# Optimization experiments

Measured on AMD Instinct MI355X. Metric: run time of the kernel, lower is better.

The kernel has to match this reference:

```python
import jax, jax.numpy as jnp
import numpy as np

HEADS = 8
HEAD_DIM = 64
INNER = HEADS * HEAD_DIM  # 512
DIM = 512
B, H, W = 8, 32, 32
KV_LEN, KV_DIM = 77, 1024


def group_norm(x, g, b, groups=32, eps=1e-6):
    # x: [B, C, H, W]
    Bx, C, Hx, Wx = x.shape
    xr = x.reshape(Bx, groups, C // groups, Hx, Wx)
    mu = xr.mean(axis=(2, 3, 4), keepdims=True)
    var = xr.var(axis=(2, 3, 4), keepdims=True)
    xr = (xr - mu) * jax.lax.rsqrt(var + eps)
    return xr.reshape(Bx, C, Hx, Wx) * g[None, :, None, None] + b[None, :, None, None]


def layer_norm(x, g, b, eps=1e-5):
    mu = x.mean(axis=-1, keepdims=True)
    var = x.var(axis=-1, keepdims=True)
    return (x - mu) * jax.lax.rsqrt(var + eps) * g + b


def attention(qx, kvx, Wq, Wk, Wv, Wo, bo):
    # qx: [B, Sq, dim_q], kvx: [B, Sk, dim_kv]
    q = qx @ Wq
    k = kvx @ Wk
    v = kvx @ Wv
    Bx, Sq, _ = q.shape
    Sk = k.shape[1]
    q = q.reshape(Bx, Sq, HEADS, HEAD_DIM)
    k = k.reshape(Bx, Sk, HEADS, HEAD_DIM)
    v = v.reshape(Bx, Sk, HEADS, HEAD_DIM)
    att = jnp.einsum('bqhd,bkhd->bhqk', q, k) * (HEAD_DIM ** -0.5)
    att = jax.nn.softmax(att.astype(jnp.float32), axis=-1).astype(q.dtype)
    o = jnp.einsum('bhqk,bkhd->bqhd', att, v).reshape(Bx, Sq, INNER)
    return o @ Wo + bo


def setup_inputs() -> dict:
    key = jax.random.key(0)
    ks = jax.random.split(key, 20)
    s = 0.02
    def n(k, shape):
        return jax.random.normal(k, shape, jnp.float32) * s
    return {
        'q': jax.random.normal(ks[0], (B, DIM, H, W), jnp.float32),
        'kv': jax.random.normal(ks[1], (B, KV_LEN, KV_DIM), jnp.float32),
        'gn_g': jnp.ones((DIM,), jnp.float32), 'gn_b': jnp.zeros((DIM,), jnp.float32),
        'ln2_g': jnp.ones((INNER,), jnp.float32), 'ln2_b': jnp.zeros((INNER,), jnp.float32),
        'ln3_g': jnp.ones((INNER,), jnp.float32), 'ln3_b': jnp.zeros((INNER,), jnp.float32),
        'ln4_g': jnp.ones((INNER,), jnp.float32), 'ln4_b': jnp.zeros((INNER,), jnp.float32),
        'fc_in_w': n(ks[2], (DIM, INNER)), 'fc_in_b': jnp.zeros((INNER,), jnp.float32),
        'fc_out_w': n(ks[3], (INNER, DIM)), 'fc_out_b': jnp.zeros((DIM,), jnp.float32),
        'a1_q': n(ks[4], (INNER, INNER)), 'a1_k': n(ks[5], (INNER, INNER)),
        'a1_v': n(ks[6], (INNER, INNER)), 'a1_o': n(ks[7], (INNER, INNER)),
        'a1_ob': jnp.zeros((INNER,), jnp.float32),
        'a2_q': n(ks[8], (INNER, INNER)), 'a2_k': n(ks[9], (KV_DIM, INNER)),
        'a2_v': n(ks[10], (KV_DIM, INNER)), 'a2_o': n(ks[11], (INNER, INNER)),
        'a2_ob': jnp.zeros((INNER,), jnp.float32),
        'ff_proj_w': n(ks[12], (INNER, INNER * 8)), 'ff_proj_b': jnp.zeros((INNER * 8,), jnp.float32),
        'ff_out_w': n(ks[13], (INNER * 4, INNER)), 'ff_out_b': jnp.zeros((INNER,), jnp.float32),
    }


def reference(q, kv, gn_g, gn_b, ln2_g, ln2_b, ln3_g, ln3_b, ln4_g, ln4_b,
              fc_in_w, fc_in_b, fc_out_w, fc_out_b,
              a1_q, a1_k, a1_v, a1_o, a1_ob,
              a2_q, a2_k, a2_v, a2_o, a2_ob,
              ff_proj_w, ff_proj_b, ff_out_w, ff_out_b):
    res = q
    Bx, C, Hx, Wx = q.shape
    x = group_norm(q, gn_g, gn_b)
    x = x.reshape(Bx, C, Hx * Wx).transpose(0, 2, 1)  # [B, S, C]
    x = x @ fc_in_w + fc_in_b
    t = layer_norm(x, ln2_g, ln2_b)
    x = attention(t, t, a1_q, a1_k, a1_v, a1_o, a1_ob) + x
    x = attention(layer_norm(x, ln3_g, ln3_b), kv, a2_q, a2_k, a2_v, a2_o, a2_ob) + x
    h = layer_norm(x, ln4_g, ln4_b) @ ff_proj_w + ff_proj_b
    a, gate = jnp.split(h, 2, axis=-1)
    x = (a * jax.nn.gelu(gate, approximate=False)) @ ff_out_w + ff_out_b + x
    x = x @ fc_out_w + fc_out_b
    x = x.transpose(0, 2, 1).reshape(Bx, C, Hx, Wx)
    return x + res
```

## Files before the change

### kernel.cpp

```cpp
#include <hip/hip_runtime.h>
#include <cstdint>
#include <cstddef>

typedef __attribute__((ext_vector_type(8))) short bf16x8;
typedef __attribute__((ext_vector_type(4))) short short4v;
typedef __attribute__((ext_vector_type(4))) float f32x4;

__device__ __forceinline__ short f2b(float f) {
    unsigned u = __builtin_bit_cast(unsigned, f);
    u = (u + 0x7FFFu + ((u >> 16) & 1u)) >> 16;
    return (short)u;
}
__device__ __forceinline__ float b2f(short s) {
    unsigned u = ((unsigned)(unsigned short)s) << 16;
    return __builtin_bit_cast(float, u);
}

__device__ __forceinline__ void gload16(const short* g, short* l) {
    __builtin_amdgcn_global_load_lds(
        (const __attribute__((address_space(1))) unsigned int*)g,
        (__attribute__((address_space(3))) unsigned int*)l, 16, 0, 0);
}

__device__ __forceinline__ float gelu_fast(float g) {
    float g2 = g * g;
    float gp = g * (0.7978845608f + 0.0356774081f * g2);
    float t = exp2f(-2.885390082f * gp);
    return g / (1.f + t);
}

__device__ __forceinline__ int pn_ffp(int n) {
    int m = (n < 2048) ? n : (n - 2048);
    int gofs = (n < 2048) ? 0 : 32;
    int x = m >> 6, c = m & 63;
    return x * 128 + ((c >> 5) << 6) + gofs + (c & 31);
}

struct PrepArgs {
    const float* src[12];
    short* dst[12];
    const float* kv;
    short* kvb;
    const float* fb;
    float* bp;
    const float* qin;
    const float* gng;
    const float* gnb;
    float* gnsc;
    float* gnsh;
};

__global__ __launch_bounds__(256) void prep(PrepArgs a) {
    int t = blockIdx.x;
    int tid = threadIdx.x;
    __shared__ float tile[32][33];
    if (t >= 6144) {
        if (t >= 6468) {
            int bb = (t - 6468) >> 5, gg = (t - 6468) & 31;
            const float4* src = (const float4*)(a.qin + ((size_t)(bb * 512 + gg * 16)) * 1024);
            float s = 0.f, s2 = 0.f;
#pragma unroll
            for (int i = 0; i < 16; ++i) {
                float4 v = src[tid + 256 * i];
                s += (v.x + v.y) + (v.z + v.w);
                s2 += (v.x * v.x + v.y * v.y) + (v.z * v.z + v.w * v.w);
            }
#pragma unroll
            for (int m = 1; m < 64; m <<= 1) {
                s += __shfl_xor(s, m);
                s2 += __shfl_xor(s2, m);
            }
            float* red = &tile[0][0];
            int wv = tid >> 6;
            if ((tid & 63) == 0) { red[wv] = s; red[4 + wv] = s2; }
            __syncthreads();
            if (tid < 16) {
                float S = red[0] + red[1] + red[2] + red[3];
                float S2 = red[4] + red[5] + red[6] + red[7];
                float mu = S * (1.f / 16384.f);
                float var = S2 * (1.f / 16384.f) - mu * mu;
                float rs = rsqrtf(var + 1e-6f);
                int c = gg * 16 + tid;
                float scale = rs * a.gng[c];
                a.gnsc[bb * 512 + c] = scale;
                a.gnsh[bb * 512 + c] = a.gnb[c] - mu * scale;
            }
            return;
        }
        if (t >= 6452) {
            int n = (t - 6452) * 256 + tid;
            if (n < 4096) a.bp[pn_ffp(n)] = a.fb[n];
            return;
        }
        int idx = (t - 6144) * 256 + tid;
        if (idx >= 78848) return;
        const float4* s = (const float4*)a.kv + (size_t)idx * 2;
        float4 va = s[0], vb = s[1];
        bf16x8 w;
        w[0] = f2b(va.x); w[1] = f2b(va.y); w[2] = f2b(va.z); w[3] = f2b(va.w);
        w[4] = f2b(vb.x); w[5] = f2b(vb.y); w[6] = f2b(vb.z); w[7] = f2b(vb.w);
        *(bf16x8*)(a.kvb + (size_t)idx * 8) = w;
        return;
    }
    const int jstart[12] = {0, 256, 512, 768, 1024, 1280, 1536, 1792, 2304, 2816, 3072, 5120};
    const int jK[12] = {512, 512, 512, 512, 512, 512, 512, 1024, 1024, 512, 512, 2048};
    const int jN[12] = {512, 512, 512, 512, 512, 512, 512, 512, 512, 512, 4096, 512};
    int j = 11;
#pragma unroll
    for (int i = 11; i >= 1; --i)
        if (t < jstart[i]) j = i - 1;
    int tx = t - jstart[j];
    int K = jK[j], N = jN[j];
    int tn = N >> 5;
    int n0 = (tx % tn) * 32, k0 = (tx / tn) * 32;
    const float* w = a.src[j];
    short* wt = a.dst[j];
    bool perm = (j == 10);

    int cx = tid & 31, ty0 = tid >> 5;
#pragma unroll
    for (int i = 0; i < 4; ++i) {
        int r = ty0 + i * 8;
        tile[r][cx] = w[(size_t)(k0 + r) * N + n0 + cx];
    }
    __syncthreads();
    int r = tid >> 3;
    int kg = (tid & 7) * 4;
    int drow = perm ? pn_ffp(n0 + r) : (n0 + r);
    short4v o = {f2b(tile[kg][r]), f2b(tile[kg + 1][r]),
                 f2b(tile[kg + 2][r]), f2b(tile[kg + 3][r])};
    *(short4v*)&wt[(size_t)drow * K + k0 + kg] = o;
}

__global__ __launch_bounds__(256) void gn_apply(const float* __restrict__ q,
                                                const float* __restrict__ sc,
                                                const float* __restrict__ sh,
                                                short* __restrict__ out) {
    __shared__ short tile[512][33];
    int b = blockIdx.x >> 5, st = blockIdx.x & 31;
    int s0 = st * 32;
    int sl = threadIdx.x & 31, cg = threadIdx.x >> 5;
    for (int c = cg; c < 512; c += 8) {
        float v = q[((size_t)(b * 512 + c)) * 1024 + s0 + sl];
        float y = v * sc[b * 512 + c] + sh[b * 512 + c];
        tile[c][sl] = f2b(y);
    }
    __syncthreads();
    int sr = threadIdx.x >> 3, ch = threadIdx.x & 7;
    short* orow = out + ((size_t)(b * 1024 + s0 + sr)) * 512;
    for (int c8 = ch * 64; c8 < ch * 64 + 64; c8 += 8) {
        bf16x8 o;
#pragma unroll
        for (int jj = 0; jj < 8; ++jj) o[jj] = tile[c8 + jj][sr];
        *(bf16x8*)&orow[c8] = o;
    }
}

__global__ __launch_bounds__(256) void ln_rows(const short* __restrict__ x,
                                               const float* __restrict__ g,
                                               const float* __restrict__ bta,
                                               short* __restrict__ out) {
    int row = blockIdx.x * 4 + (threadIdx.x >> 6);
    int lane = threadIdx.x & 63;
    bf16x8 v8 = *(const bf16x8*)(x + (size_t)row * 512 + lane * 8);
    float v[8];
#pragma unroll
    for (int j = 0; j < 8; ++j) v[j] = b2f(v8[j]);
    float s = 0.f, s2 = 0.f;
#pragma unroll
    for (int j = 0; j < 8; ++j) { s += v[j]; s2 += v[j] * v[j]; }
#pragma unroll
    for (int m = 1; m < 64; m <<= 1) {
        s += __shfl_xor(s, m);
        s2 += __shfl_xor(s2, m);
    }
    float mu = s * (1.f / 512.f);
    float var = s2 * (1.f / 512.f) - mu * mu;
    float rs = rsqrtf(var + 1e-5f);
    float4 ga = ((const float4*)g)[lane * 2], gb = ((const float4*)g)[lane * 2 + 1];
    float4 ba = ((const float4*)bta)[lane * 2], bb = ((const float4*)bta)[lane * 2 + 1];
    bf16x8 o;
    o[0] = f2b((v[0] - mu) * rs * ga.x + ba.x);
    o[1] = f2b((v[1] - mu) * rs * ga.y + ba.y);
    o[2] = f2b((v[2] - mu) * rs * ga.z + ba.z);
    o[3] = f2b((v[3] - mu) * rs * ga.w + ba.w);
    o[4] = f2b((v[4] - mu) * rs * gb.x + bb.x);
    o[5] = f2b((v[5] - mu) * rs * gb.y + bb.y);
    o[6] = f2b((v[6] - mu) * rs * gb.z + bb.z);
    o[7] = f2b((v[7] - mu) * rs * gb.w + bb.w);
    *(bf16x8*)(out + (size_t)row * 512 + lane * 8) = o;
}

template <int BN>
__device__ __forceinline__ void gemm_body(
    short* smem,
    const short* __restrict__ A, const short* __restrict__ BT,
    int M, int N, int K,
    const float* __restrict__ bias,
    const short* __restrict__ addSrcB,
    short* __restrict__ outB,
    const float* __restrict__ resid,
    float* __restrict__ outFinal,
    int mode, int bx, int by) {
    constexpr int FJ = BN / 32;
    constexpr int ASZ = 3 * 128 * 32;
    short* Asb = smem;
    short* Bsb = smem + ASZ;
    int tid = threadIdx.x;
    int wave = tid >> 6, lane = tid & 63;
    int wr = wave >> 1, wc = wave & 1;
    int m0 = by * 128, n0 = bx * BN;
    f32x4 acc[4][FJ];
#pragma unroll
    for (int i = 0; i < 4; ++i)
#pragma unroll
        for (int j = 0; j < FJ; ++j) acc[i][j] = (f32x4){0.f, 0.f, 0.f, 0.f};

    int srow = tid >> 2;
    int scg = (((tid & 3) ^ ((tid >> 3) & 3)) << 3);
    int ar0 = m0 + srow; if (ar0 >= M) ar0 = M - 1;
    int ar1 = m0 + 64 + srow; if (ar1 >= M) ar1 = M - 1;
    const short* ag0 = A + (size_t)ar0 * K + scg;
    const short* ag1 = A + (size_t)ar1 * K + scg;
    const short* bg0 = BT + (size_t)(n0 + srow) * K + scg;
    const short* bg1 = BT + (size_t)(n0 + 64 + srow) * K + scg;
    int nk = K >> 5;

    auto stage = [&](int buf) {
        gload16(ag0, &Asb[buf * 4096 + wave * 512]);
        gload16(ag1, &Asb[buf * 4096 + 2048 + wave * 512]);
        gload16(bg0, &Bsb[buf * (BN * 32) + wave * 512]);
        if constexpr (BN == 128) gload16(bg1, &Bsb[buf * 4096 + 2048 + wave * 512]);
        ag0 += 32; ag1 += 32; bg0 += 32; bg1 += 32;
    };
    stage(0);
    stage(1);

    int lr = lane & 15, g = lane >> 4;

#define GL_STEP(KT, BUF)                                                          \
    {                                                                             \
        __builtin_amdgcn_sched_barrier(0);                                        \
        if ((KT) + 1 < nk) {                                                      \
            if constexpr (BN == 128)                                              \
                asm volatile("s_waitcnt vmcnt(4)" ::: "memory");                  \
            else                                                                  \
                asm volatile("s_waitcnt vmcnt(3)" ::: "memory");                  \
        } else {                                                                  \
            asm volatile("s_waitcnt vmcnt(0)" ::: "memory");                      \
        }                                                                         \
        __builtin_amdgcn_sched_barrier(0);                                        \
        __builtin_amdgcn_s_barrier();                                             \
        if ((KT) + 2 < nk) stage(((BUF) + 2) % 3);                                \
        bf16x8 af[4], bfr[FJ];                                                    \
        _Pragma("unroll") for (int i = 0; i < 4; ++i) {                           \
            int row = wr * 64 + i * 16 + lr;                                      \
            af[i] = *(const bf16x8*)&Asb[(BUF) * 4096 + row * 32 +                \
                                         ((g ^ ((row >> 1) & 3)) << 3)];          \
        }                                                                         \
        _Pragma("unroll") for (int j = 0; j < FJ; ++j) {                          \
            int row = wc * (BN / 2) + j * 16 + lr;                                \
            bfr[j] = *(const bf16x8*)&Bsb[(BUF) * (BN * 32) + row * 32 +          \
                                          ((g ^ ((row >> 1) & 3)) << 3)];         \
        }                                                                         \
        _Pragma("unroll") for (int i = 0; i < 4; ++i)                             \
            _Pragma("unroll") for (int j = 0; j < FJ; ++j)                        \
                acc[i][j] = __builtin_amdgcn_mfma_f32_16x16x32_bf16(              \
                    af[i], bfr[j], acc[i][j], 0, 0, 0);                           \
    }

    for (int kt = 0; kt < nk; kt += 3) {
        GL_STEP(kt, 0);
        if (kt + 1 < nk) GL_STEP(kt + 1, 1);
        if (kt + 2 < nk) GL_STEP(kt + 2, 2);
    }
#undef GL_STEP

    int lq = lane >> 4;
    if (mode == 1) {
#pragma unroll
        for (int i = 0; i < 4; ++i)
#pragma unroll
            for (int j = 0; j < FJ; ++j) {
                int mm0 = m0 + wr * 64 + i * 16 + lq * 4;
                int nn = n0 + wc * (BN / 2) + j * 16 + lr;
                int bb = mm0 >> 10, ss = mm0 & 1023;
                size_t oi = ((size_t)(bb * 512 + nn)) * 1024 + ss;
                float bv = bias ? bias[nn] : 0.f;
                float4 rv = *(const float4*)&resid[oi];
                float4 ov;
                ov.x = acc[i][j][0] + bv + rv.x;
                ov.y = acc[i][j][1] + bv + rv.y;
                ov.z = acc[i][j][2] + bv + rv.z;
                ov.w = acc[i][j][3] + bv + rv.w;
                *(float4*)&outFinal[oi] = ov;
            }
        return;
    }
    {
        constexpr int EC = BN + 4;
        float* ef = (float*)smem;
#pragma unroll
        for (int h = 0; h < 2; ++h) {
            __syncthreads();
            if (wr == h) {
#pragma unroll
                for (int i = 0; i < 4; ++i)
#pragma unroll
                    for (int j = 0; j < FJ; ++j)
#pragma unroll
                        for (int r = 0; r < 4; ++r)
                            ef[(i * 16 + lq * 4 + r) * EC + wc * (BN / 2) + j * 16 + lr] =
                                acc[i][j][r];
            }
            __syncthreads();
#pragma unroll
            for (int q = 0; q < BN / 16; ++q) {
                int idx = q * 256 + tid;
                int row = idx / (BN / 4);
                int cq = (idx % (BN / 4)) * 4;
                int mm = m0 + h * 64 + row;
                if (mm >= M) continue;
                int nn = n0 + cq;
                float4 v = *(float4*)&ef[row * EC + cq];
                if (bias) {
                    float4 b4 = *(const float4*)&bias[nn];
                    v.x += b4.x; v.y += b4.y; v.z += b4.z; v.w += b4.w;
                }
                size_t ig = (size_t)mm * N + nn;
                if (addSrcB) {
                    short4v a4 = *(const short4v*)&addSrcB[ig];
                    v.x += b2f(a4[0]); v.y += b2f(a4[1]);
                    v.z += b2f(a4[2]); v.w += b2f(a4[3]);
                }
                short4v o = {f2b(v.x), f2b(v.y), f2b(v.z), f2b(v.w)};
                *(short4v*)&outB[ig] = o;
            }
        }
    }
}

template <int BN>
__global__ __launch_bounds__(256, 1) void gemm_gl(
    const short* __restrict__ A, const short* __restrict__ BT,
    int M, int N, int K,
    const float* __restrict__ bias,
    const short* __restrict__ addSrcB,
    short* __restrict__ outB,
    const float* __restrict__ resid,
    float* __restrict__ outFinal,
    int mode) {
    __shared__ __attribute__((aligned(16))) short smem[3 * 128 * 32 + 3 * BN * 32];
    gemm_body<BN>(smem, A, BT, M, N, K, bias, addSrcB, outB, resid, outFinal,
                  mode, blockIdx.x, blockIdx.y);
}

__global__ __launch_bounds__(256, 1) void gemm_dual(
    const short* __restrict__ A1, const short* __restrict__ B1,
    short* __restrict__ O1, int M1, int N1, int K1,
    const short* __restrict__ A2, const short* __restrict__ B2,
    short* __restrict__ O2, int M2, int N2, int K2) {
    __shared__ __attribute__((aligned(16))) short smem[3 * 128 * 32 + 3 * 128 * 32];
    int t = blockIdx.x;
    if (t < 80) {
        gemm_body<64>(smem, A2, B2, M2, N2, K2, nullptr, nullptr, O2,
                      nullptr, nullptr, 0, t & 15, t >> 4);
    } else {
        t -= 80;
        gemm_body<128>(smem, A1, B1, M1, N1, K1, nullptr, nullptr, O1,
                       nullptr, nullptr, 0, t & 3, t >> 2);
    }
}

__global__ __launch_bounds__(512, 1) void gemm256w(
    const short* __restrict__ A, const short* __restrict__ BT,
    int M, int N, int K,
    const float* __restrict__ bias,
    const short* __restrict__ addSrcB,
    short* __restrict__ outB,
    int mode) {
    __shared__ __attribute__((aligned(16))) short smem[3 * 4096 + 3 * 8192];
    short* Asb = smem;
    short* Bsb = smem + 12288;
    int tid = threadIdx.x;
    int wave = tid >> 6, lane = tid & 63;
    int wrM = wave >> 2, wcN = wave & 3;
    int m0 = blockIdx.y * 128, n0 = blockIdx.x * 256;
    f32x4 acc[4][4];
#pragma unroll
    for (int i = 0; i < 4; ++i)
#pragma unroll
        for (int j = 0; j < 4; ++j) acc[i][j] = (f32x4){0.f, 0.f, 0.f, 0.f};

    const short* gp[3];
    int ldsoff[3];
    bool isA[3];
#pragma unroll
    for (int s = 0; s < 3; ++s) {
        int qq = wave * 3 + s;
        bool a = qq < 8;
        int r = (a ? qq : qq - 8) * 16 + (lane >> 2);
        int sc = (((lane & 3) ^ ((r >> 1) & 3)) << 3);
        gp[s] = a ? (A + (size_t)(m0 + r) * K + sc)
                  : (BT + (size_t)(n0 + r) * K + sc);
        ldsoff[s] = (a ? qq : (qq - 8)) * 512;
        isA[s] = a;
    }
    int nk = K >> 5;
    auto stage = [&](int buf) {
#pragma unroll
        for (int s = 0; s < 3; ++s) {
            short* l = isA[s] ? &Asb[buf * 4096 + ldsoff[s]]
                              : &Bsb[buf * 8192 + ldsoff[s]];
            gload16(gp[s], l);
            gp[s] += 32;
        }
    };
    stage(0);
    stage(1);

    int lr = lane & 15, g = lane >> 4;

#define W8_STEP(KT, BUF)                                                          \
    {                                                                             \
        __builtin_amdgcn_sched_barrier(0);                                        \
        if ((KT) + 1 < nk) {                                                      \
            asm volatile("s_waitcnt vmcnt(3)" ::: "memory");                      \
        } else {                                                                  \
            asm volatile("s_waitcnt vmcnt(0)" ::: "memory");                      \
        }                                                                         \
        __builtin_amdgcn_sched_barrier(0);                                        \
        __builtin_amdgcn_s_barrier();                                             \
        if ((KT) + 2 < nk) stage(((BUF) + 2) % 3);                                \
        bf16x8 af[4], bfr[4];                                                     \
        _Pragma("unroll") for (int i = 0; i < 4; ++i) {                           \
            int row = wrM * 64 + i * 16 + lr;                                     \
            af[i] = *(const bf16x8*)&Asb[(BUF) * 4096 + row * 32 +                \
                                         ((g ^ ((row >> 1) & 3)) << 3)];          \
        }                                                                         \
        _Pragma("unroll") for (int j = 0; j < 4; ++j) {                           \
            int row = wcN * 64 + j * 16 + lr;                                     \
            bfr[j] = *(const bf16x8*)&Bsb[(BUF) * 8192 + row * 32 +               \
                                          ((g ^ ((row >> 1) & 3)) << 3)];         \
        }                                                                         \
        _Pragma("unroll") for (int i = 0; i < 4; ++i)                             \
            _Pragma("unroll") for (int j = 0; j < 4; ++j)                         \
                acc[i][j] = __builtin_amdgcn_mfma_f32_16x16x32_bf16(              \
                    af[i], bfr[j], acc[i][j], 0, 0, 0);                           \
    }

    for (int kt = 0; kt < nk; kt += 3) {
        W8_STEP(kt, 0);
        if (kt + 1 < nk) W8_STEP(kt + 1, 1);
        if (kt + 2 < nk) W8_STEP(kt + 2, 2);
    }
#undef W8_STEP

    int lq = lane >> 4;
    if (mode == 2) {
        short* eb = smem;
        int xhalf = wcN >> 1, half = wcN & 1;
        __syncthreads();
#pragma unroll
        for (int i = 0; i < 4; ++i)
#pragma unroll
            for (int j = 0; j < 2; ++j)
#pragma unroll
                for (int r = 0; r < 4; ++r) {
                    int slot = n0 + wcN * 64 + j * 16 + lr;
                    float a = acc[i][j][r] + bias[slot];
                    float gt = acc[i][j + 2][r] + bias[slot + 32];
                    float ge = gelu_fast(gt);
                    int row = wrM * 64 + i * 16 + lq * 4 + r;
                    int col = xhalf * 64 + half * 32 + j * 16 + lr;
                    eb[row * 136 + col] = f2b(a * ge);
                }
        __syncthreads();
#pragma unroll
        for (int q = 0; q < 4; ++q) {
            int idx = q * 512 + tid;
            int row = idx >> 4, cg = (idx & 15) * 8;
            bf16x8 o = *(bf16x8*)&eb[row * 136 + cg];
            *(bf16x8*)&outB[(size_t)(m0 + row) * 2048 + blockIdx.x * 128 + cg] = o;
        }
        return;
    }
    {
        float* ef = (float*)smem;
#pragma unroll
        for (int h = 0; h < 2; ++h) {
            __syncthreads();
            if (wrM == h) {
#pragma unroll
                for (int i = 0; i < 4; ++i)
#pragma unroll
                    for (int j = 0; j < 4; ++j)
#pragma unroll
                        for (int r = 0; r < 4; ++r)
                            ef[(i * 16 + lq * 4 + r) * 260 + wcN * 64 + j * 16 + lr] =
                                acc[i][j][r];
            }
            __syncthreads();
#pragma unroll
            for (int q = 0; q < 8; ++q) {
                int idx = q * 512 + tid;
                int row = idx >> 6;
                int cq = (idx & 63) * 4;
                float4 v = *(float4*)&ef[row * 260 + cq];
                int nn = n0 + cq;
                if (bias) {
                    float4 b4 = *(const float4*)&bias[nn];
                    v.x += b4.x; v.y += b4.y; v.z += b4.z; v.w += b4.w;
                }
                size_t ig = (size_t)(m0 + h * 64 + row) * N + nn;
                if (addSrcB) {
                    short4v a4 = *(const short4v*)&addSrcB[ig];
                    v.x += b2f(a4[0]); v.y += b2f(a4[1]);
                    v.z += b2f(a4[2]); v.w += b2f(a4[3]);
                }
                short4v o = {f2b(v.x), f2b(v.y), f2b(v.z), f2b(v.w)};
                *(short4v*)&outB[ig] = o;
            }
        }
    }
}

__global__ __launch_bounds__(256, 1) void attn_mfma(const short* __restrict__ qp,
                                                    const short* __restrict__ kp,
                                                    const short* __restrict__ vp,
                                                    short* __restrict__ op,
                                                    int kv_len, int kvBatchRows,
                                                    int qStride, int kvStride) {
    __shared__ __attribute__((aligned(16))) short Kt[64][72];
    __shared__ __attribute__((aligned(16))) short Vt[64][72];
    __shared__ __attribute__((aligned(16))) short Pt[4][2][16][72];
    int tid = threadIdx.x, w = tid >> 6, lane = tid & 63;
    int g = lane >> 4, c = lane & 15;
    int id = blockIdx.x;
    int xcd = id & 7, jj2 = id >> 3;
    int bh = xcd * 8 + (jj2 >> 3);
    int qtile = jj2 & 7;
    int b = bh >> 3, h = bh & 7;
    int q0 = qtile * 128 + w * 16;

    const float QS = 0.125f * 1.44269504f;
    bf16x8 qa[2][2];
#pragma unroll
    for (int qi = 0; qi < 2; ++qi) {
        const short* qbase = qp + ((size_t)(b * 1024 + q0 + qi * 64 + c)) * qStride + h * 64;
        bf16x8 qr0 = *(const bf16x8*)(qbase + g * 8);
        bf16x8 qr1 = *(const bf16x8*)(qbase + 32 + g * 8);
#pragma unroll
        for (int j = 0; j < 8; ++j) {
            qa[qi][0][j] = f2b(b2f(qr0[j]) * QS);
            qa[qi][1][j] = f2b(b2f(qr1[j]) * QS);
        }
    }
    bf16x8 vones;
#pragma unroll
    for (int j = 0; j < 8; ++j) vones[j] = (short)0x3F80;

    f32x4 oac[2][4], oacl[2];
#pragma unroll
    for (int qi = 0; qi < 2; ++qi) {
#pragma unroll
        for (int dt = 0; dt < 4; ++dt) oac[qi][dt] = (f32x4){0.f, 0.f, 0.f, 0.f};
        oacl[qi] = (f32x4){0.f, 0.f, 0.f, 0.f};
    }

    int skey = tid & 63, sd0 = (tid >> 6) * 16;
    int ntile = (kv_len + 63) >> 6;
    size_t kvbase = (size_t)b * kvBatchRows;

    bf16x8 k0, k1, v0, v1;
    {
        int krow = skey < kv_len ? skey : kv_len - 1;
        const short* kpp = kp + (kvbase + krow) * kvStride + h * 64 + sd0;
        const short* vpp = vp + (kvbase + krow) * kvStride + h * 64 + sd0;
        k0 = *(const bf16x8*)kpp; k1 = *(const bf16x8*)(kpp + 8);
        v0 = *(const bf16x8*)vpp; v1 = *(const bf16x8*)(vpp + 8);
    }

    for (int kt = 0; kt < ntile; ++kt) {
        __syncthreads();
        *(bf16x8*)&Kt[skey][sd0] = k0;
        *(bf16x8*)&Kt[skey][sd0 + 8] = k1;
#pragma unroll
        for (int j = 0; j < 8; ++j) {
            Vt[sd0 + j][skey] = v0[j];
            Vt[sd0 + 8 + j][skey] = v1[j];
        }
        __syncthreads();
        if (kt + 1 < ntile) {
            int krow = (kt + 1) * 64 + skey;
            if (krow >= kv_len) krow = kv_len - 1;
            const short* kpp = kp + (kvbase + krow) * kvStride + h * 64 + sd0;
            const short* vpp = vp + (kvbase + krow) * kvStride + h * 64 + sd0;
            k0 = *(const bf16x8*)kpp; k1 = *(const bf16x8*)(kpp + 8);
            v0 = *(const bf16x8*)vpp; v1 = *(const bf16x8*)(vpp + 8);
        }

        f32x4 s[2][4];
        __builtin_amdgcn_s_setprio(1);
#pragma unroll
        for (int nt = 0; nt < 4; ++nt) {
            bf16x8 kb0 = *(const bf16x8*)&Kt[nt * 16 + c][g * 8];
            bf16x8 kb1 = *(const bf16x8*)&Kt[nt * 16 + c][32 + g * 8];
#pragma unroll
            for (int qi = 0; qi < 2; ++qi) {
                s[qi][nt] = __builtin_amdgcn_mfma_f32_16x16x32_bf16(
                    qa[qi][0], kb0, (f32x4){0.f, 0.f, 0.f, 0.f}, 0, 0, 0);
                s[qi][nt] = __builtin_amdgcn_mfma_f32_16x16x32_bf16(
                    qa[qi][1], kb1, s[qi][nt], 0, 0, 0);
            }
        }
        __builtin_amdgcn_s_setprio(0);
        if (kt * 64 + 64 > kv_len) {
#pragma unroll
            for (int nt = 0; nt < 4; ++nt) {
                bool valid = kt * 64 + nt * 16 + c < kv_len;
#pragma unroll
                for (int qi = 0; qi < 2; ++qi)
#pragma unroll
                    for (int r = 0; r < 4; ++r)
                        s[qi][nt][r] = valid ? exp2f(s[qi][nt][r]) : 0.f;
            }
        } else {
#pragma unroll
            for (int nt = 0; nt < 4; ++nt)
#pragma unroll
                for (int qi = 0; qi < 2; ++qi)
#pragma unroll
                    for (int r = 0; r < 4; ++r)
                        s[qi][nt][r] = exp2f(s[qi][nt][r]);
        }

        bf16x8 pa[2][2];
#pragma unroll
        for (int qi = 0; qi < 2; ++qi) {
#pragma unroll
            for (int nt = 0; nt < 4; ++nt)
#pragma unroll
                for (int r = 0; r < 4; ++r)
                    Pt[w][qi][4 * g + r][nt * 16 + c] = f2b(s[qi][nt][r]);
        }
#pragma unroll
        for (int qi = 0; qi < 2; ++qi) {
            pa[qi][0] = *(const bf16x8*)&Pt[w][qi][c][g * 8];
            pa[qi][1] = *(const bf16x8*)&Pt[w][qi][c][32 + g * 8];
        }
        __builtin_amdgcn_s_setprio(1);
#pragma unroll
        for (int dt = 0; dt < 4; ++dt) {
            bf16x8 vb0 = *(const bf16x8*)&Vt[dt * 16 + c][g * 8];
            bf16x8 vb1 = *(const bf16x8*)&Vt[dt * 16 + c][32 + g * 8];
#pragma unroll
            for (int qi = 0; qi < 2; ++qi) {
                oac[qi][dt] = __builtin_amdgcn_mfma_f32_16x16x32_bf16(pa[qi][0], vb0, oac[qi][dt], 0, 0, 0);
                oac[qi][dt] = __builtin_amdgcn_mfma_f32_16x16x32_bf16(pa[qi][1], vb1, oac[qi][dt], 0, 0, 0);
            }
        }
#pragma unroll
        for (int qi = 0; qi < 2; ++qi) {
            oacl[qi] = __builtin_amdgcn_mfma_f32_16x16x32_bf16(pa[qi][0], vones, oacl[qi], 0, 0, 0);
            oacl[qi] = __builtin_amdgcn_mfma_f32_16x16x32_bf16(pa[qi][1], vones, oacl[qi], 0, 0, 0);
        }
        __builtin_amdgcn_s_setprio(0);
    }

#pragma unroll
    for (int qi = 0; qi < 2; ++qi)
#pragma unroll
        for (int r = 0; r < 4; ++r) {
            float inv = 1.f / oacl[qi][r];
            short* orow = op + ((size_t)(b * 1024 + q0 + qi * 64 + 4 * g + r)) * 512 + h * 64;
#pragma unroll
            for (int dt = 0; dt < 4; ++dt)
                orow[dt * 16 + c] = f2b(oac[qi][dt][r] * inv);
        }
}

extern "C" void kernel_launch(void* const* d_in, const int* in_sizes, int n_in,
                              void* d_out, int out_size, void* d_ws, size_t ws_size,
                              hipStream_t stream) {
    (void)in_sizes; (void)n_in; (void)out_size; (void)ws_size;
    const float* q_in = (const float*)d_in[0];
    const float* kv_in = (const float*)d_in[1];
    const float* gn_g = (const float*)d_in[2];
    const float* gn_b = (const float*)d_in[3];
    const float* ln2_g = (const float*)d_in[4];
    const float* ln2_b = (const float*)d_in[5];
    const float* ln3_g = (const float*)d_in[6];
    const float* ln3_b = (const float*)d_in[7];
    const float* ln4_g = (const float*)d_in[8];
    const float* ln4_b = (const float*)d_in[9];
    const float* fc_in_w = (const float*)d_in[10];
    const float* fc_in_b = (const float*)d_in[11];
    const float* fc_out_w = (const float*)d_in[12];
    const float* fc_out_b = (const float*)d_in[13];
    const float* a1_qw = (const float*)d_in[14];
    const float* a1_kw = (const float*)d_in[15];
    const float* a1_vw = (const float*)d_in[16];
    const float* a1_ow = (const float*)d_in[17];
    const float* a1_ob = (const float*)d_in[18];
    const float* a2_qw = (const float*)d_in[19];
    const float* a2_kw = (const float*)d_in[20];
    const float* a2_vw = (const float*)d_in[21];
    const float* a2_ow = (const float*)d_in[22];
    const float* a2_ob = (const float*)d_in[23];
    const float* ffp_w = (const float*)d_in[24];
    const float* ffp_b = (const float*)d_in[25];
    const float* ffo_w = (const float*)d_in[26];
    const float* ffo_b = (const float*)d_in[27];
    float* out = (float*)d_out;

    char* p = (char*)d_ws;
    auto alloc = [&](size_t n) {
        char* r = p;
        p += (n + 255) & ~(size_t)255;
        return r;
    };
    short* wt_fci = (short*)alloc((size_t)512 * 512 * 2);
    short* wt_fco = (short*)alloc((size_t)512 * 512 * 2);
    short* wt_qkv = (short*)alloc((size_t)1536 * 512 * 2);
    short* wt_a1o = (short*)alloc((size_t)512 * 512 * 2);
    short* wt_a2q = (short*)alloc((size_t)512 * 512 * 2);
    short* wt_kv2 = (short*)alloc((size_t)1024 * 1024 * 2);
    short* wt_a2o = (short*)alloc((size_t)512 * 512 * 2);
    short* wt_ffp = (short*)alloc((size_t)4096 * 512 * 2);
    short* wt_ffo = (short*)alloc((size_t)512 * 2048 * 2);
    float* biasP = (float*)alloc((size_t)4096 * 4);
    short* xb = (short*)alloc((size_t)8192 * 512 * 2);
    short* tb = (short*)alloc((size_t)8192 * 512 * 2);
    short* qkvbuf = (short*)alloc((size_t)8192 * 1536 * 2);
    short* qbuf = (short*)alloc((size_t)8192 * 512 * 2);
    short* kvpbuf = (short*)alloc((size_t)616 * 1024 * 2);
    short* obuf = (short*)alloc((size_t)8192 * 512 * 2);
    short* kvb = (short*)alloc((size_t)616 * 1024 * 2);
    short* ggb = (short*)alloc((size_t)8192 * 2048 * 2);
    float* gnsc = (float*)alloc((size_t)8 * 512 * 4);
    float* gnsh = (float*)alloc((size_t)8 * 512 * 4);

    PrepArgs pa;
    pa.src[0] = fc_in_w;  pa.dst[0] = wt_fci;
    pa.src[1] = fc_out_w; pa.dst[1] = wt_fco;
    pa.src[2] = a1_qw;    pa.dst[2] = wt_qkv;
    pa.src[3] = a1_kw;    pa.dst[3] = wt_qkv + (size_t)512 * 512;
    pa.src[4] = a1_vw;    pa.dst[4] = wt_qkv + (size_t)1024 * 512;
    pa.src[5] = a1_ow;    pa.dst[5] = wt_a1o;
    pa.src[6] = a2_qw;    pa.dst[6] = wt_a2q;
    pa.src[7] = a2_kw;    pa.dst[7] = wt_kv2;
    pa.src[8] = a2_vw;    pa.dst[8] = wt_kv2 + (size_t)512 * 1024;
    pa.src[9] = a2_ow;    pa.dst[9] = wt_a2o;
    pa.src[10] = ffp_w;   pa.dst[10] = wt_ffp;
    pa.src[11] = ffo_w;   pa.dst[11] = wt_ffo;
    pa.kv = kv_in; pa.kvb = kvb; pa.fb = ffp_b; pa.bp = biasP;
    pa.qin = q_in; pa.gng = gn_g; pa.gnb = gn_b; pa.gnsc = gnsc; pa.gnsh = gnsh;
    prep<<<6724, 256, 0, stream>>>(pa);

    gn_apply<<<256, 256, 0, stream>>>(q_in, gnsc, gnsh, tb);
    gemm_gl<128><<<dim3(4, 64), 256, 0, stream>>>(
        tb, wt_fci, 8192, 512, 512, fc_in_b, nullptr, xb, nullptr, nullptr, 0);
    ln_rows<<<2048, 256, 0, stream>>>(xb, ln2_g, ln2_b, tb);
    gemm_gl<128><<<dim3(12, 64), 256, 0, stream>>>(
        tb, wt_qkv, 8192, 1536, 512, nullptr, nullptr, qkvbuf, nullptr, nullptr, 0);
    attn_mfma<<<512, 256, 0, stream>>>(qkvbuf, qkvbuf + 512, qkvbuf + 1024, obuf,
                                       1024, 1024, 1536, 1536);
    gemm_gl<128><<<dim3(4, 64), 256, 0, stream>>>(
        obuf, wt_a1o, 8192, 512, 512, a1_ob, xb, xb, nullptr, nullptr, 0);
    ln_rows<<<2048, 256, 0, stream>>>(xb, ln3_g, ln3_b, tb);
    gemm_dual<<<336, 256, 0, stream>>>(tb, wt_a2q, qbuf, 8192, 512, 512,
                                       kvb, wt_kv2, kvpbuf, 616, 1024, 1024);
    attn_mfma<<<512, 256, 0, stream>>>(qbuf, kvpbuf, kvpbuf + 512, obuf,
                                       77, 77, 512, 1024);
    gemm_gl<128><<<dim3(4, 64), 256, 0, stream>>>(
        obuf, wt_a2o, 8192, 512, 512, a2_ob, xb, xb, nullptr, nullptr, 0);
    ln_rows<<<2048, 256, 0, stream>>>(xb, ln4_g, ln4_b, tb);
    gemm256w<<<dim3(16, 64), 512, 0, stream>>>(tb, wt_ffp, 8192, 4096, 512,
                                               biasP, nullptr, ggb, 2);
    gemm_gl<128><<<dim3(4, 64), 256, 0, stream>>>(
        ggb, wt_ffo, 8192, 512, 2048, ffo_b, xb, tb, nullptr, nullptr, 0);
    gemm_gl<128><<<dim3(4, 64), 256, 0, stream>>>(
        tb, wt_fco, 8192, 512, 512, fc_out_b, nullptr, nullptr, q_in, out, 1);
}
```

Baseline: 274.2 us.

## Replace FF projection GEMM with 256x256-tile specialized GeGLU kernel

Replaces the generic 128x256 FF-projection GEMM with a kernel specialised for K=512 and the GeGLU epilogue. Each block now computes a 256x256 tile with 8x4 accumulators per wave, uses a 64-wide K step double-buffered in 128KB of LDS with an XOR swizzle, and splits the inner loop into four MFMA phases with s_setprio and barriers between them. The larger tile raises operand reuse and halves the block count. In exchange it needs more registers and LDS, drops to a two-stage buffer with a full vmcnt(0) wait each step, and hardcodes the K=512 and N=2048 strides.

```diff
diff --git a/kernel.cpp b/kernel.cpp
--- a/kernel.cpp
+++ b/kernel.cpp
@@ -372,156 +372,138 @@
     }
 }
 
-__global__ __launch_bounds__(512, 1) void gemm256w(
+__global__ __launch_bounds__(512, 1) void gemm8p(
     const short* __restrict__ A, const short* __restrict__ BT,
-    int M, int N, int K,
-    const float* __restrict__ bias,
-    const short* __restrict__ addSrcB,
-    short* __restrict__ outB,
-    int mode) {
-    __shared__ __attribute__((aligned(16))) short smem[3 * 4096 + 3 * 8192];
-    short* Asb = smem;
-    short* Bsb = smem + 12288;
+    const float* __restrict__ bias, short* __restrict__ outB) {
+    __shared__ __attribute__((aligned(16))) short smem[65536];
     int tid = threadIdx.x;
     int wave = tid >> 6, lane = tid & 63;
     int wrM = wave >> 2, wcN = wave & 3;
-    int m0 = blockIdx.y * 128, n0 = blockIdx.x * 256;
-    f32x4 acc[4][4];
-#pragma unroll
-    for (int i = 0; i < 4; ++i)
-#pragma unroll
-        for (int j = 0; j < 4; ++j) acc[i][j] = (f32x4){0.f, 0.f, 0.f, 0.f};
-
-    const short* gp[3];
-    int ldsoff[3];
-    bool isA[3];
-#pragma unroll
-    for (int s = 0; s < 3; ++s) {
-        int qq = wave * 3 + s;
-        bool a = qq < 8;
-        int r = (a ? qq : qq - 8) * 16 + (lane >> 2);
-        int sc = (((lane & 3) ^ ((r >> 1) & 3)) << 3);
-        gp[s] = a ? (A + (size_t)(m0 + r) * K + sc)
-                  : (BT + (size_t)(n0 + r) * K + sc);
-        ldsoff[s] = (a ? qq : (qq - 8)) * 512;
-        isA[s] = a;
-    }
-    int nk = K >> 5;
-    auto stage = [&](int buf) {
-#pragma unroll
-        for (int s = 0; s < 3; ++s) {
-            short* l = isA[s] ? &Asb[buf * 4096 + ldsoff[s]]
-                              : &Bsb[buf * 8192 + ldsoff[s]];
-            gload16(gp[s], l);
-            gp[s] += 32;
-        }
+    int m0 = blockIdx.y * 256, n0 = blockIdx.x * 256;
+    f32x4 acc[8][4];
+#pragma unroll
+    for (int m = 0; m < 8; ++m)
+#pragma unroll
+        for (int n = 0; n < 4; ++n) acc[m][n] = (f32x4){0.f, 0.f, 0.f, 0.f};
+
+    int rA = tid >> 3;
+    int cxor = ((tid & 7) ^ (rA & 7)) * 8;
+    const short* ag = A + (size_t)(m0 + rA) * 512 + cxor;
+    const short* bg = BT + (size_t)(n0 + rA) * 512 + cxor;
+
+    auto stage = [&](int t, int buf) {
+        int ko = t * 64;
+#pragma unroll
+        for (int o = 0; o < 4; ++o)
+            gload16(ag + (size_t)o * 32768 + ko,
+                    &smem[buf * 32768 + o * 4096 + wave * 512]);
+#pragma unroll
+        for (int o = 0; o < 4; ++o)
+            gload16(bg + (size_t)o * 32768 + ko,
+                    &smem[buf * 32768 + 16384 + o * 4096 + wave * 512]);
     };
-    stage(0);
-    stage(1);
+    stage(0, 0);
 
     int lr = lane & 15, g = lane >> 4;
-
-#define W8_STEP(KT, BUF)                                                          \
-    {                                                                             \
-        __builtin_amdgcn_sched_barrier(0);                                        \
-        if ((KT) + 1 < nk) {                                                      \
-            asm volatile("s_waitcnt vmcnt(3)" ::: "memory");                      \
-        } else {                                                                  \
-            asm volatile("s_waitcnt vmcnt(0)" ::: "memory");                      \
-        }                                                                         \
-        __builtin_amdgcn_sched_barrier(0);                                        \
-        __builtin_amdgcn_s_barrier();                                             \
-        if ((KT) + 2 < nk) stage(((BUF) + 2) % 3);                                \
-        bf16x8 af[4], bfr[4];                                                     \
-        _Pragma("unroll") for (int i = 0; i < 4; ++i) {                           \
-            int row = wrM * 64 + i * 16 + lr;                                     \
-            af[i] = *(const bf16x8*)&Asb[(BUF) * 4096 + row * 32 +                \
-                                         ((g ^ ((row >> 1) & 3)) << 3)];          \
-        }                                                                         \
-        _Pragma("unroll") for (int j = 0; j < 4; ++j) {                           \
-            int row = wcN * 64 + j * 16 + lr;                                     \
-            bfr[j] = *(const bf16x8*)&Bsb[(BUF) * 8192 + row * 32 +               \
-                                          ((g ^ ((row >> 1) & 3)) << 3)];         \
-        }                                                                         \
-        _Pragma("unroll") for (int i = 0; i < 4; ++i)                             \
-            _Pragma("unroll") for (int j = 0; j < 4; ++j)                         \
-                acc[i][j] = __builtin_amdgcn_mfma_f32_16x16x32_bf16(              \
-                    af[i], bfr[j], acc[i][j], 0, 0, 0);                           \
-    }
-
-    for (int kt = 0; kt < nk; kt += 3) {
-        W8_STEP(kt, 0);
-        if (kt + 1 < nk) W8_STEP(kt + 1, 1);
-        if (kt + 2 < nk) W8_STEP(kt + 2, 2);
-    }
-#undef W8_STEP
-
+    int ach[2][8], bch[2][4];
+#pragma unroll
+    for (int ks = 0; ks < 2; ++ks) {
+#pragma unroll
+        for (int m = 0; m < 8; ++m) {
+            int row = wrM * 128 + m * 16 + lr;
+            ach[ks][m] = row * 64 + (((ks * 4 + g) ^ (row & 7)) << 3);
+        }
+#pragma unroll
+        for (int n = 0; n < 4; ++n) {
+            int row = wcN * 64 + n * 16 + lr;
+            bch[ks][n] = 16384 + row * 64 + (((ks * 4 + g) ^ (row & 7)) << 3);
+        }
+    }
+
+    const int nt = 8;
+    for (int t = 0; t < nt; ++t) {
+        int buf = t & 1;
+        __builtin_amdgcn_sched_barrier(0);
+        asm volatile("s_waitcnt vmcnt(0)" ::: "memory");
+        __builtin_amdgcn_sched_barrier(0);
+        __builtin_amdgcn_s_barrier();
+        const short* Lb = &smem[buf * 32768];
+        bf16x8 bf0[4], bf1[4], af[4];
+        if (t + 1 < nt) stage(t + 1, buf ^ 1);
+#pragma unroll
+        for (int n = 0; n < 4; ++n) bf0[n] = *(const bf16x8*)&Lb[bch[0][n]];
+#pragma unroll
+        for (int m = 0; m < 4; ++m) af[m] = *(const bf16x8*)&Lb[ach[0][m]];
+        __builtin_amdgcn_s_setprio(1);
+#pragma unroll
+        for (int m = 0; m < 4; ++m)
+#pragma unroll
+            for (int n = 0; n < 4; ++n)
+                acc[m][n] = __builtin_amdgcn_mfma_f32_16x16x32_bf16(
+                    af[m], bf0[n], acc[m][n], 0, 0, 0);
+        __builtin_amdgcn_s_setprio(0);
+        __builtin_amdgcn_s_barrier();
+#pragma unroll
+        for (int n = 0; n < 4; ++n) bf1[n] = *(const bf16x8*)&Lb[bch[1][n]];
+#pragma unroll
+        for (int m = 0; m < 4; ++m) af[m] = *(const bf16x8*)&Lb[ach[1][m]];
+        __builtin_amdgcn_s_setprio(1);
+#pragma unroll
+        for (int m = 0; m < 4; ++m)
+#pragma unroll
+            for (int n = 0; n < 4; ++n)
+                acc[m][n] = __builtin_amdgcn_mfma_f32_16x16x32_bf16(
+                    af[m], bf1[n], acc[m][n], 0, 0, 0);
+        __builtin_amdgcn_s_setprio(0);
+        __builtin_amdgcn_s_barrier();
+#pragma unroll
+        for (int m = 0; m < 4; ++m) af[m] = *(const bf16x8*)&Lb[ach[0][m + 4]];
+        __builtin_amdgcn_s_setprio(1);
+#pragma unroll
+        for (int m = 0; m < 4; ++m)
+#pragma unroll
+            for (int n = 0; n < 4; ++n)
+                acc[m + 4][n] = __builtin_amdgcn_mfma_f32_16x16x32_bf16(
+                    af[m], bf0[n], acc[m + 4][n], 0, 0, 0);
+        __builtin_amdgcn_s_setprio(0);
+        __builtin_amdgcn_s_barrier();
+#pragma unroll
+        for (int m = 0; m < 4; ++m) af[m] = *(const bf16x8*)&Lb[ach[1][m + 4]];
+        __builtin_amdgcn_s_setprio(1);
+#pragma unroll
+        for (int m = 0; m < 4; ++m)
+#pragma unroll
+            for (int n = 0; n < 4; ++n)
+                acc[m + 4][n] = __builtin_amdgcn_mfma_f32_16x16x32_bf16(
+                    af[m], bf1[n], acc[m + 4][n], 0, 0, 0);
+        __builtin_amdgcn_s_setprio(0);
+    }
+
+    __syncthreads();
+    short* eb = smem;
     int lq = lane >> 4;
-    if (mode == 2) {
-        short* eb = smem;
-        int xhalf = wcN >> 1, half = wcN & 1;
-        __syncthreads();
-#pragma unroll
-        for (int i = 0; i < 4; ++i)
-#pragma unroll
-            for (int j = 0; j < 2; ++j)
-#pragma unroll
-                for (int r = 0; r < 4; ++r) {
-                    int slot = n0 + wcN * 64 + j * 16 + lr;
-                    float a = acc[i][j][r] + bias[slot];
-                    float gt = acc[i][j + 2][r] + bias[slot + 32];
-                    float ge = gelu_fast(gt);
-                    int row = wrM * 64 + i * 16 + lq * 4 + r;
-                    int col = xhalf * 64 + half * 32 + j * 16 + lr;
-                    eb[row * 136 + col] = f2b(a * ge);
-                }
-        __syncthreads();
-#pragma unroll
-        for (int q = 0; q < 4; ++q) {
-            int idx = q * 512 + tid;
-            int row = idx >> 4, cg = (idx & 15) * 8;
-            bf16x8 o = *(bf16x8*)&eb[row * 136 + cg];
-            *(bf16x8*)&outB[(size_t)(m0 + row) * 2048 + blockIdx.x * 128 + cg] = o;
-        }
-        return;
-    }
-    {
-        float* ef = (float*)smem;
-#pragma unroll
-        for (int h = 0; h < 2; ++h) {
-            __syncthreads();
-            if (wrM == h) {
-#pragma unroll
-                for (int i = 0; i < 4; ++i)
-#pragma unroll
-                    for (int j = 0; j < 4; ++j)
-#pragma unroll
-                        for (int r = 0; r < 4; ++r)
-                            ef[(i * 16 + lq * 4 + r) * 260 + wcN * 64 + j * 16 + lr] =
-                                acc[i][j][r];
-            }
-            __syncthreads();
-#pragma unroll
-            for (int q = 0; q < 8; ++q) {
-                int idx = q * 512 + tid;
-                int row = idx >> 6;
-                int cq = (idx & 63) * 4;
-                float4 v = *(float4*)&ef[row * 260 + cq];
-                int nn = n0 + cq;
-                if (bias) {
-                    float4 b4 = *(const float4*)&bias[nn];
-                    v.x += b4.x; v.y += b4.y; v.z += b4.z; v.w += b4.w;
-                }
-                size_t ig = (size_t)(m0 + h * 64 + row) * N + nn;
-                if (addSrcB) {
-                    short4v a4 = *(const short4v*)&addSrcB[ig];
-                    v.x += b2f(a4[0]); v.y += b2f(a4[1]);
-                    v.z += b2f(a4[2]); v.w += b2f(a4[3]);
-                }
-                short4v o = {f2b(v.x), f2b(v.y), f2b(v.z), f2b(v.w)};
-                *(short4v*)&outB[ig] = o;
-            }
-        }
+    int xhalf = wcN >> 1, half = wcN & 1;
+#pragma unroll
+    for (int m = 0; m < 8; ++m)
+#pragma unroll
+        for (int n = 0; n < 2; ++n)
+#pragma unroll
+            for (int r = 0; r < 4; ++r) {
+                int slot = n0 + wcN * 64 + n * 16 + lr;
+                float a = acc[m][n][r] + bias[slot];
+                float gt = acc[m][n + 2][r] + bias[slot + 32];
+                float ge = gelu_fast(gt);
+                int row = wrM * 128 + m * 16 + lq * 4 + r;
+                int col = xhalf * 64 + half * 32 + n * 16 + lr;
+                eb[row * 136 + col] = f2b(a * ge);
+            }
+    __syncthreads();
+#pragma unroll
+    for (int q = 0; q < 8; ++q) {
+        int idx = q * 512 + tid;
+        int row = idx >> 4, cg = (idx & 15) * 8;
+        bf16x8 o = *(bf16x8*)&eb[row * 136 + cg];
+        *(bf16x8*)&outB[(size_t)(m0 + row) * 2048 + blockIdx.x * 128 + cg] = o;
     }
 }
 
@@ -776,8 +758,7 @@
     gemm_gl<128><<<dim3(4, 64), 256, 0, stream>>>(
         obuf, wt_a2o, 8192, 512, 512, a2_ob, xb, xb, nullptr, nullptr, 0);
     ln_rows<<<2048, 256, 0, stream>>>(xb, ln4_g, ln4_b, tb);
-    gemm256w<<<dim3(16, 64), 512, 0, stream>>>(tb, wt_ffp, 8192, 4096, 512,
-                                               biasP, nullptr, ggb, 2);
+    gemm8p<<<dim3(16, 32), 512, 0, stream>>>(tb, wt_ffp, biasP, ggb);
     gemm_gl<128><<<dim3(4, 64), 256, 0, stream>>>(
         ggb, wt_ffo, 8192, 512, 2048, ffo_b, xb, tb, nullptr, nullptr, 0);
     gemm_gl<128><<<dim3(4, 64), 256, 0, stream>>>(
```

After: 281.4 us. 2.6% more time.
